# Optimization experiments

Hardware: AMD Instinct MI355X
Metric: run time of the kernel (lower is better)

The kernel has to match this reference:

```python
import jax, jax.numpy as jnp
import numpy as np

B, N, E, HD = 4, 2048, 2048, 128
E2 = 2 * E
EPS = 1e-6


def setup_inputs() -> dict:
    key = jax.random.key(0)
    ks = jax.random.split(key, 7)
    s = 0.02  # init_std
    return {
        "x": jax.random.normal(ks[0], (B, N, E), dtype=jnp.float32),
        "Wq1": jax.random.normal(ks[1], (E, HD), dtype=jnp.float32) * s,
        "Wq2": jax.random.normal(ks[2], (HD, E2), dtype=jnp.float32) * s,
        "Wk1": jax.random.normal(ks[3], (E, HD), dtype=jnp.float32) * s,
        "Wk2": jax.random.normal(ks[4], (HD, E2), dtype=jnp.float32) * s,
        "Wv": jax.random.normal(ks[5], (E, E2), dtype=jnp.float32) * s,
        "Wo": jax.random.normal(ks[6], (E2, E), dtype=jnp.float32) * s,
        "norm_w": jnp.ones((E2,), dtype=jnp.float32),
    }


def reference(x, Wq1, Wq2, Wk1, Wk2, Wv, Wo, norm_w):
    # low-rank factored projections: embed -> head_dim -> 2*embed
    q = jax.nn.silu((x @ Wq1) @ Wq2)          # [B,N,2E]
    log_f_raw = (x @ Wk1) @ Wk2                # [B,N,2E]
    v = x @ Wv                                 # [B,N,2E]

    # faithful to source (lower_bound is None branch):
    # f = sigmoid(raw); log_f = logsigmoid(f); k = 1 - exp(log_f)
    f = jax.nn.sigmoid(log_f_raw)
    log_f = jax.nn.log_sigmoid(f)
    a = jnp.exp(log_f)                         # decay (forget gate)
    k = 1.0 - a                                # input gate

    # HGRN-1 elementwise gated recurrence: h_t = a_t*h_{t-1} + k_t*v_t
    def combine(c1, c2):
        a1, b1 = c1
        a2, b2 = c2
        return (a1 * a2, a2 * b1 + b2)

    _, h = jax.lax.associative_scan(combine, (a, k * v), axis=1)
    out = q * h                                # [B,N,2E]

    # RMSNorm over channel dim (2E)
    out = out * jax.lax.rsqrt(jnp.mean(out * out, axis=-1, keepdims=True) + EPS)
    out = out * norm_w

    return out @ Wo                            # [B,N,E]
```

## Files before the change

kernel.cpp:

```cpp
#include <hip/hip_runtime.h>


typedef unsigned short u16;
typedef __attribute__((ext_vector_type(4))) float f32x4;
typedef __attribute__((ext_vector_type(8))) __bf16 bf16x8;
typedef __attribute__((ext_vector_type(8))) u16 u16x8;
typedef __attribute__((ext_vector_type(4))) unsigned int u32x4;

__device__ __forceinline__ float bf2f(u16 u) {
  unsigned int i = ((unsigned int)u) << 16;
  return __builtin_bit_cast(float, i);
}
__device__ __forceinline__ u16 f2bf(float f) {
  unsigned int i = __builtin_bit_cast(unsigned int, f);
  i += 0x7fffu + ((i >> 16) & 1u);
  return (u16)(i >> 16);
}

__device__ __forceinline__ void gload_lds16(const u16* g, u16* l) {
  __builtin_amdgcn_global_load_lds(
      (const __attribute__((address_space(1))) void*)g,
      (__attribute__((address_space(3))) void*)l, 16, 0, 0);
}

__global__ __launch_bounds__(256) void cast_kernel(const float* __restrict__ in,
                                                   u16* __restrict__ out, long n) {
  long i = ((long)blockIdx.x * 256 + threadIdx.x) * 4;
  if (i >= n) return;
  f32x4 fv = *(const f32x4*)&in[i];
  unsigned long long pk = (unsigned long long)f2bf(fv[0]) |
                          ((unsigned long long)f2bf(fv[1]) << 16) |
                          ((unsigned long long)f2bf(fv[2]) << 32) |
                          ((unsigned long long)f2bf(fv[3]) << 48);
  *(unsigned long long*)&out[i] = pk;
}

__global__ __launch_bounds__(256) void transpose_cast(const float* __restrict__ W,
                                                      u16* __restrict__ WT, int R, int Cc) {
  __shared__ float tile[32][33];
  const int tx = threadIdx.x, ty = threadIdx.y;
  const int x = blockIdx.x * 32 + tx;
  const int ybase = blockIdx.y * 32;
#pragma unroll
  for (int i = 0; i < 32; i += 8)
    tile[ty + i][tx] = W[(size_t)(ybase + ty + i) * Cc + x];
  __syncthreads();
  const int xt = ybase + tx;
  const int ytbase = blockIdx.x * 32;
#pragma unroll
  for (int i = 0; i < 32; i += 8)
    WT[(size_t)(ytbase + ty + i) * R + xt] = f2bf(tile[tx][ty + i]);
}

__global__ __launch_bounds__(256) void transpose_cast_nw(const float* __restrict__ W,
                                                         const float* __restrict__ nw,
                                                         u16* __restrict__ WT, int R, int Cc) {
  __shared__ float tile[32][33];
  const int tx = threadIdx.x, ty = threadIdx.y;
  const int x = blockIdx.x * 32 + tx;
  const int ybase = blockIdx.y * 32;
#pragma unroll
  for (int i = 0; i < 32; i += 8)
    tile[ty + i][tx] = W[(size_t)(ybase + ty + i) * Cc + x];
  __syncthreads();
  const int xt = ybase + tx;
  const float s = nw[xt];
  const int ytbase = blockIdx.x * 32;
#pragma unroll
  for (int i = 0; i < 32; i += 8)
    WT[(size_t)(ytbase + ty + i) * R + xt] = f2bf(tile[tx][ty + i] * s);
}

template <int EPI>
__global__ __launch_bounds__(256) void gemm_bt(const u16* __restrict__ A, int lda,
                                               const u16* __restrict__ BT,
                                               void* __restrict__ Cv,
                                               int M, int N, int K) {
  __shared__ __align__(16) u16 As[4096];
  __shared__ __align__(16) u16 Bs[4096];
  const int tid = threadIdx.x;
  const int lane = tid & 63;
  const int wid = tid >> 6;
  const int wr = wid >> 1, wc = wid & 1;
  const long bm = (long)blockIdx.x * 128;
  const long bn = (long)blockIdx.y * 128;

  const int sm = lane >> 2;
  const int sk = (lane & 3) << 3;
  const u16* Ag0 = A + (size_t)(bm + wid * 16 + sm) * lda + sk;
  const u16* Ag1 = A + (size_t)(bm + 64 + wid * 16 + sm) * lda + sk;
  const u16* Bg0 = BT + (size_t)(bn + wid * 16 + sm) * K + sk;
  const u16* Bg1 = BT + (size_t)(bn + 64 + wid * 16 + sm) * K + sk;
  u16* As0 = As + wid * 512;
  u16* As1 = As + 2048 + wid * 512;
  u16* Bs0 = Bs + wid * 512;
  u16* Bs1 = Bs + 2048 + wid * 512;

  f32x4 acc[4][4] = {};

  const int fra = wr * 64 + (lane & 15);
  const int frb = wc * 64 + (lane & 15);
  const int kg = (lane >> 4) << 3;

  for (int kk = 0; kk < K; kk += 32) {
    gload_lds16(Ag0 + kk, As0);
    gload_lds16(Ag1 + kk, As1);
    gload_lds16(Bg0 + kk, Bs0);
    gload_lds16(Bg1 + kk, Bs1);
    __syncthreads();
    bf16x8 af[4], bv[4];
#pragma unroll
    for (int mi = 0; mi < 4; ++mi)
      af[mi] = *reinterpret_cast<const bf16x8*>(&As[(fra + mi * 16) * 32 + kg]);
#pragma unroll
    for (int ni = 0; ni < 4; ++ni)
      bv[ni] = *reinterpret_cast<const bf16x8*>(&Bs[(frb + ni * 16) * 32 + kg]);
#pragma unroll
    for (int mi = 0; mi < 4; ++mi) {
#pragma unroll
      for (int ni = 0; ni < 4; ++ni)
        acc[mi][ni] =
            __builtin_amdgcn_mfma_f32_16x16x32_bf16(af[mi], bv[ni], acc[mi][ni], 0, 0, 0);
    }
    __syncthreads();
  }

  const int r0 = wr * 64 + ((lane >> 4) << 2);
  const int c0 = wc * 64 + (lane & 15);
#pragma unroll
  for (int mi = 0; mi < 4; ++mi) {
#pragma unroll
    for (int ni = 0; ni < 4; ++ni) {
#pragma unroll
      for (int r = 0; r < 4; ++r) {
        size_t row = (size_t)(bm + r0 + mi * 16 + r);
        size_t col = (size_t)(bn + c0 + ni * 16);
        size_t idx = row * (size_t)N + col;
        float val = acc[mi][ni][r];
        if constexpr (EPI == 0) {
          ((u16*)Cv)[idx] = f2bf(val);
        } else if constexpr (EPI == 2) {
          float f = 1.f / (1.f + __expf(-val));
          float aa = 1.f / (1.f + __expf(-f));
          ((u16*)Cv)[idx] = f2bf(aa);
        } else {
          float hv = bf2f(((u16*)Cv)[idx]);
          float s = 1.f / (1.f + __expf(-val));
          ((u16*)Cv)[idx] = f2bf(val * s * hv);
        }
      }
    }
  }
}

template <int EPI>
__global__ __launch_bounds__(512, 2) void gemm8(const u16* __restrict__ A,
                                                const u16* __restrict__ BT,
                                                void* __restrict__ Cv,
                                                const float* __restrict__ RS,
                                                int M, int N, int K, int nby) {
  __shared__ __align__(16) u16 lds_[4][2][256][32];
  const int tid = threadIdx.x;
  const int lane = tid & 63;
  const int w = tid >> 6;
  const int wr = w >> 2;
  const int wc = w & 3;

  const int nwg = gridDim.x;
  const int bid = blockIdx.x;
  const int swz = (bid & 7) * (nwg >> 3) + (bid >> 3);
  const long bm = (long)(swz / nby) * 256;
  const long bn = (long)(swz % nby) * 256;

  const int srow = lane >> 2;
  const int scol = ((lane & 3) ^ ((lane >> 3) & 3)) << 3;
  const u16* Ag = A + (size_t)(bm + w * 32 + srow) * K + scol;
  const u16* Bg = BT + (size_t)(bn + w * 32 + srow) * K + scol;

#define STG_A(t)                                                     \
  {                                                                  \
    const u16* s_ = Ag + (size_t)(t) * 32;                           \
    u16* d_ = &lds_[(t) & 3][0][w * 32][0];                          \
    gload_lds16(s_, d_);                                             \
    gload_lds16(s_ + (size_t)16 * K, d_ + 512);                      \
  }
#define STG_B(t)                                                     \
  {                                                                  \
    const u16* s_ = Bg + (size_t)(t) * 32;                           \
    u16* d_ = &lds_[(t) & 3][1][w * 32][0];                          \
    gload_lds16(s_, d_);                                             \
    gload_lds16(s_ + (size_t)16 * K, d_ + 512);                      \
  }

  const int frow = lane & 15;
  const int colw = (((lane >> 4) ^ ((frow >> 1) & 3)) << 3);

  f32x4 acc[8][4] = {};

  const int NT = K >> 5;
  STG_A(0); STG_B(0);
  STG_A(1); STG_B(1);
  STG_A(2); STG_B(2);

  for (int u = 0; u < NT; ++u) {
    if (u <= NT - 3)      asm volatile("s_waitcnt vmcnt(8)" ::: "memory");
    else if (u == NT - 2) asm volatile("s_waitcnt vmcnt(4)" ::: "memory");
    else                  asm volatile("s_waitcnt vmcnt(0)" ::: "memory");
    __builtin_amdgcn_s_barrier();
    if (u + 3 < NT) { STG_A(u + 3); STG_B(u + 3); }

    const u16* LA = &lds_[u & 3][0][0][0];
    const u16* LB = &lds_[u & 3][1][0][0];
    bf16x8 a0[4], b0[4], a1[4];
#pragma unroll
    for (int i = 0; i < 4; ++i)
      a0[i] = *reinterpret_cast<const bf16x8*>(&LA[(wr * 128 + i * 16 + frow) * 32 + colw]);
#pragma unroll
    for (int i = 0; i < 4; ++i)
      b0[i] = *reinterpret_cast<const bf16x8*>(&LB[(wc * 64 + i * 16 + frow) * 32 + colw]);
    __builtin_amdgcn_s_setprio(1);
#pragma unroll
    for (int i = 0; i < 4; ++i)
#pragma unroll
      for (int j = 0; j < 4; ++j)
        acc[i][j] = __builtin_amdgcn_mfma_f32_16x16x32_bf16(a0[i], b0[j], acc[i][j], 0, 0, 0);
    __builtin_amdgcn_s_setprio(0);
#pragma unroll
    for (int i = 0; i < 4; ++i)
      a1[i] = *reinterpret_cast<const bf16x8*>(&LA[(wr * 128 + 64 + i * 16 + frow) * 32 + colw]);
    __builtin_amdgcn_s_setprio(1);
#pragma unroll
    for (int i = 0; i < 4; ++i)
#pragma unroll
      for (int j = 0; j < 4; ++j)
        acc[4 + i][j] = __builtin_amdgcn_mfma_f32_16x16x32_bf16(a1[i], b0[j], acc[4 + i][j], 0, 0, 0);
    __builtin_amdgcn_s_setprio(0);
  }

  const int er = (lane >> 4) << 2;
  const int ec = lane & 15;
#pragma unroll
  for (int mf = 0; mf < 8; ++mf) {
#pragma unroll
    for (int r = 0; r < 4; ++r) {
      const size_t row = (size_t)(bm + wr * 128 + mf * 16 + er + r);
      float rscale = 1.f;
      if constexpr (EPI == 3) rscale = RS[row];
#pragma unroll
      for (int nf = 0; nf < 4; ++nf) {
        const size_t col = (size_t)(bn + wc * 64 + nf * 16 + ec);
        const size_t idx = row * (size_t)N + col;
        const float val = acc[mf][nf][r];
        if constexpr (EPI == 0) {
          ((u16*)Cv)[idx] = f2bf(val);
        } else {
          ((float*)Cv)[idx] = val * rscale;
        }
      }
    }
  }
#undef STG_A
#undef STG_B
}

__global__ __launch_bounds__(256) void scan_a(const u16* __restrict__ a,
                                              const u16* __restrict__ v,
                                              float* __restrict__ S_p,
                                              float* __restrict__ S_h) {
  const int idx = blockIdx.x * 256 + threadIdx.x;
  const int ch8 = idx & 511;
  const int c = (idx >> 9) & 31;
  const int b = idx >> 14;
  const int ch = ch8 << 3;
  size_t off = ((size_t)(b * 2048 + c * 64)) * 4096 + ch;
  float h[8], p[8];
#pragma unroll
  for (int j = 0; j < 8; ++j) { h[j] = 0.f; p[j] = 1.f; }
  for (int t = 0; t < 64; ++t) {
    u16x8 ua = *(const u16x8*)&a[off];
    u16x8 uv = *(const u16x8*)&v[off];
#pragma unroll
    for (int j = 0; j < 8; ++j) {
      float at = bf2f(ua[j]);
      h[j] = at * h[j] + (1.f - at) * bf2f(uv[j]);
      p[j] *= at;
    }
    off += 4096;
  }
  size_t so = (size_t)(b * 32 + c) * 4096 + ch;
#pragma unroll
  for (int j = 0; j < 8; ++j) { S_p[so + j] = p[j]; S_h[so + j] = h[j]; }
}

__global__ __launch_bounds__(256) void scan_b(const float* __restrict__ S_p,
                                              const float* __restrict__ S_h,
                                              float* __restrict__ Hin) {
  const int idx = blockIdx.x * 256 + threadIdx.x;
  const int b = idx >> 12;
  const int ch = idx & 4095;
  float H = 0.f;
  for (int c = 0; c < 32; ++c) {
    size_t so = (size_t)(b * 32 + c) * 4096 + ch;
    Hin[so] = H;
    H = S_p[so] * H + S_h[so];
  }
}

__global__ __launch_bounds__(256) void scan_c(const u16* __restrict__ a,
                                              u16* __restrict__ vh,
                                              const float* __restrict__ Hin) {
  const int idx = blockIdx.x * 256 + threadIdx.x;
  const int ch8 = idx & 511;
  const int c = (idx >> 9) & 31;
  const int b = idx >> 14;
  const int ch = ch8 << 3;
  size_t so = (size_t)(b * 32 + c) * 4096 + ch;
  float h[8];
#pragma unroll
  for (int j = 0; j < 8; ++j) h[j] = Hin[so + j];
  size_t off = ((size_t)(b * 2048 + c * 64)) * 4096 + ch;
  for (int t = 0; t < 64; ++t) {
    u16x8 ua = *(const u16x8*)&a[off];
    u16x8 uv = *(const u16x8*)&vh[off];
    u16x8 out;
#pragma unroll
    for (int j = 0; j < 8; ++j) {
      float at = bf2f(ua[j]);
      h[j] = at * h[j] + (1.f - at) * bf2f(uv[j]);
      out[j] = f2bf(h[j]);
    }
    *(u16x8*)&vh[off] = out;
    off += 4096;
  }
}

__global__ __launch_bounds__(256) void rowssq(const u16* __restrict__ g,
                                              float* __restrict__ rs) {
  const size_t base = (size_t)blockIdx.x * 4096;
  const int tid = threadIdx.x;
  const int c0 = tid * 16;
  u16 vals[16];
  *(u32x4*)&vals[0] = *(const u32x4*)&g[base + c0];
  *(u32x4*)&vals[8] = *(const u32x4*)&g[base + c0 + 8];
  float s = 0.f;
#pragma unroll
  for (int i = 0; i < 16; ++i) {
    float f = bf2f(vals[i]);
    s += f * f;
  }
#pragma unroll
  for (int o = 32; o > 0; o >>= 1) s += __shfl_down(s, o, 64);
  __shared__ float red[4];
  if ((tid & 63) == 0) red[tid >> 6] = s;
  __syncthreads();
  if (tid == 0) {
    float tot = red[0] + red[1] + red[2] + red[3];
    rs[blockIdx.x] = rsqrtf(tot * (1.0f / 4096.0f) + 1e-6f);
  }
}

extern "C" void kernel_launch(void* const* d_in, const int* in_sizes, int n_in,
                              void* d_out, int out_size, void* d_ws, size_t ws_size,
                              hipStream_t stream) {
  const float* x   = (const float*)d_in[0];
  const float* Wq1 = (const float*)d_in[1];
  const float* Wq2 = (const float*)d_in[2];
  const float* Wk1 = (const float*)d_in[3];
  const float* Wk2 = (const float*)d_in[4];
  const float* Wv  = (const float*)d_in[5];
  const float* Wo  = (const float*)d_in[6];
  const float* nw  = (const float*)d_in[7];

  char* ws = (char*)d_ws;
  u16* X     = (u16*)(ws + 0);
  u16* WVT   = (u16*)(ws + 33554432);
  u16* AA    = (u16*)(ws + 0);
  u16* VV    = (u16*)(ws + 67108864);
  u16* T12   = (u16*)(ws + 134217728);
  u16* WQK1T = (u16*)(ws + 138412032);
  u16* WQ2T  = (u16*)(ws + 139460608);
  u16* WK2T  = (u16*)(ws + 140509184);
  u16* WOT   = (u16*)(ws + 141557760);
  float* S_P = (float*)(ws + 158334976);
  float* S_H = (float*)(ws + 160432128);
  float* HIN = (float*)(ws + 162529280);
  float* RS  = (float*)(ws + 164626432);

  cast_kernel<<<16384, 256, 0, stream>>>(x, X, 16777216L);
  transpose_cast<<<dim3(4, 64),   dim3(32, 8), 0, stream>>>(Wq1, WQK1T, 2048, 128);
  transpose_cast<<<dim3(4, 64),   dim3(32, 8), 0, stream>>>(Wk1, WQK1T + 128 * 2048, 2048, 128);
  transpose_cast<<<dim3(128, 4),  dim3(32, 8), 0, stream>>>(Wq2, WQ2T, 128, 4096);
  transpose_cast<<<dim3(128, 4),  dim3(32, 8), 0, stream>>>(Wk2, WK2T, 128, 4096);
  transpose_cast<<<dim3(128, 64), dim3(32, 8), 0, stream>>>(Wv, WVT, 2048, 4096);
  transpose_cast_nw<<<dim3(64, 128), dim3(32, 8), 0, stream>>>(Wo, nw, WOT, 4096, 2048);

  gemm_bt<0><<<dim3(64, 2), 256, 0, stream>>>(X, 2048, WQK1T, T12, 8192, 256, 2048);
  gemm8<0><<<512, 512, 0, stream>>>(X, WVT, VV, nullptr, 8192, 4096, 2048, 16);
  gemm_bt<2><<<dim3(64, 32), 256, 0, stream>>>(T12 + 128, 256, WK2T, AA, 8192, 4096, 128);

  scan_a<<<256, 256, 0, stream>>>(AA, VV, S_P, S_H);
  scan_b<<<64, 256, 0, stream>>>(S_P, S_H, HIN);
  scan_c<<<256, 256, 0, stream>>>(AA, VV, HIN);

  gemm_bt<4><<<dim3(64, 32), 256, 0, stream>>>(T12, 256, WQ2T, VV, 8192, 4096, 128);

  rowssq<<<8192, 256, 0, stream>>>(VV, RS);
  gemm8<3><<<256, 512, 0, stream>>>(VV, WOT, d_out, RS, 8192, 2048, 4096, 8);
}
```

Baseline: 659.3 us.

## Shrink gemm8 tile to 256x128 with 4 waves and triple-buffered LDS

Changes the main GEMM kernel from 512-thread 256x256 tiles with a 4-stage LDS pipeline to 256-thread 256x128 tiles with 3-stage buffering. Each wave still computes a 128x64 subtile, while the per-block LDS footprint drops, which should let more blocks fit per CU. The grid doubles for both the V projection and the output projection. In exchange, arithmetic intensity per tile falls, B loads are reused less, and prefetch depth is shallower.

```diff
diff --git a/kernel.cpp b/kernel.cpp
--- a/kernel.cpp
+++ b/kernel.cpp
@@ -154,42 +154,42 @@
 }
 
 template <int EPI>
-__global__ __launch_bounds__(512, 2) void gemm8(const u16* __restrict__ A,
+__global__ __launch_bounds__(256, 2) void gemm8(const u16* __restrict__ A,
                                                 const u16* __restrict__ BT,
                                                 void* __restrict__ Cv,
                                                 const float* __restrict__ RS,
                                                 int M, int N, int K, int nby) {
-  __shared__ __align__(16) u16 lds_[4][2][256][32];
+  __shared__ __align__(16) u16 ldsA[3][256][32];
+  __shared__ __align__(16) u16 ldsB[3][128][32];
   const int tid = threadIdx.x;
   const int lane = tid & 63;
   const int w = tid >> 6;
-  const int wr = w >> 2;
-  const int wc = w & 3;
+  const int wr = w >> 1;
+  const int wc = w & 1;
 
   const int nwg = gridDim.x;
   const int bid = blockIdx.x;
   const int swz = (bid & 7) * (nwg >> 3) + (bid >> 3);
   const long bm = (long)(swz / nby) * 256;
-  const long bn = (long)(swz % nby) * 256;
+  const long bn = (long)(swz % nby) * 128;
 
   const int srow = lane >> 2;
   const int scol = ((lane & 3) ^ ((lane >> 3) & 3)) << 3;
-  const u16* Ag = A + (size_t)(bm + w * 32 + srow) * K + scol;
-  const u16* Bg = BT + (size_t)(bn + w * 32 + srow) * K + scol;
-
-#define STG_A(t)                                                     \
-  {                                                                  \
-    const u16* s_ = Ag + (size_t)(t) * 32;                           \
-    u16* d_ = &lds_[(t) & 3][0][w * 32][0];                          \
-    gload_lds16(s_, d_);                                             \
-    gload_lds16(s_ + (size_t)16 * K, d_ + 512);                      \
-  }
-#define STG_B(t)                                                     \
-  {                                                                  \
-    const u16* s_ = Bg + (size_t)(t) * 32;                           \
-    u16* d_ = &lds_[(t) & 3][1][w * 32][0];                          \
-    gload_lds16(s_, d_);                                             \
-    gload_lds16(s_ + (size_t)16 * K, d_ + 512);                      \
+  const u16* Ag = A + (size_t)(bm + w * 16 + srow) * K + scol;
+  const u16* Bg = BT + (size_t)(bn + w * 16 + srow) * K + scol;
+
+#define STG(t)                                                        \
+  {                                                                   \
+    const u16* sa_ = Ag + (size_t)(t) * 32;                           \
+    const u16* sb_ = Bg + (size_t)(t) * 32;                           \
+    u16* da_ = &ldsA[(t) % 3][w * 16][0];                             \
+    u16* db_ = &ldsB[(t) % 3][w * 16][0];                             \
+    gload_lds16(sa_, da_);                                            \
+    gload_lds16(sa_ + (size_t)64 * K, da_ + 2048);                    \
+    gload_lds16(sa_ + (size_t)128 * K, da_ + 4096);                   \
+    gload_lds16(sa_ + (size_t)192 * K, da_ + 6144);                   \
+    gload_lds16(sb_, db_);                                            \
+    gload_lds16(sb_ + (size_t)64 * K, db_ + 2048);                    \
   }
 
   const int frow = lane & 15;
@@ -198,19 +198,16 @@
   f32x4 acc[8][4] = {};
 
   const int NT = K >> 5;
-  STG_A(0); STG_B(0);
-  STG_A(1); STG_B(1);
-  STG_A(2); STG_B(2);
+  STG(0); STG(1);
 
   for (int u = 0; u < NT; ++u) {
-    if (u <= NT - 3)      asm volatile("s_waitcnt vmcnt(8)" ::: "memory");
-    else if (u == NT - 2) asm volatile("s_waitcnt vmcnt(4)" ::: "memory");
-    else                  asm volatile("s_waitcnt vmcnt(0)" ::: "memory");
+    if (u < NT - 1) asm volatile("s_waitcnt vmcnt(6)" ::: "memory");
+    else            asm volatile("s_waitcnt vmcnt(0)" ::: "memory");
     __builtin_amdgcn_s_barrier();
-    if (u + 3 < NT) { STG_A(u + 3); STG_B(u + 3); }
-
-    const u16* LA = &lds_[u & 3][0][0][0];
-    const u16* LB = &lds_[u & 3][1][0][0];
+    if (u + 2 < NT) STG(u + 2);
+
+    const u16* LA = &ldsA[u % 3][0][0];
+    const u16* LB = &ldsB[u % 3][0][0];
     bf16x8 a0[4], b0[4], a1[4];
 #pragma unroll
     for (int i = 0; i < 4; ++i)
@@ -259,8 +256,7 @@
       }
     }
   }
-#undef STG_A
-#undef STG_B
+#undef STG
 }
 
 __global__ __launch_bounds__(256) void scan_a(const u16* __restrict__ a,
@@ -395,7 +391,7 @@
   transpose_cast_nw<<<dim3(64, 128), dim3(32, 8), 0, stream>>>(Wo, nw, WOT, 4096, 2048);
 
   gemm_bt<0><<<dim3(64, 2), 256, 0, stream>>>(X, 2048, WQK1T, T12, 8192, 256, 2048);
-  gemm8<0><<<512, 512, 0, stream>>>(X, WVT, VV, nullptr, 8192, 4096, 2048, 16);
+  gemm8<0><<<1024, 256, 0, stream>>>(X, WVT, VV, nullptr, 8192, 4096, 2048, 32);
   gemm_bt<2><<<dim3(64, 32), 256, 0, stream>>>(T12 + 128, 256, WK2T, AA, 8192, 4096, 128);
 
   scan_a<<<256, 256, 0, stream>>>(AA, VV, S_P, S_H);
@@ -405,5 +401,5 @@
   gemm_bt<4><<<dim3(64, 32), 256, 0, stream>>>(T12, 256, WQ2T, VV, 8192, 4096, 128);
 
   rowssq<<<8192, 256, 0, stream>>>(VV, RS);
-  gemm8<3><<<256, 512, 0, stream>>>(VV, WOT, d_out, RS, 8192, 2048, 4096, 8);
-}
+  gemm8<3><<<512, 256, 0, stream>>>(VV, WOT, d_out, RS, 8192, 2048, 4096, 16);
+}
```

New measurement: 692.7 us. 1.05x slower.
